# Performance work log

Measured on AMD Instinct MI355X. Metric: run time of the kernel, lower is better.

## Reference

```python
import jax, jax.numpy as jnp
import numpy as np

N_NODES = 100000
N_EDGES = 1600000
IN_FEATS = 256
OUT_FEATS = 128


def setup_inputs() -> dict:
    key = jax.random.key(0)
    k1, k2, k3, k4 = jax.random.split(key, 4)
    feat = jax.random.normal(k1, (N_NODES, IN_FEATS), dtype=jnp.float32)
    src = jax.random.randint(k2, (N_EDGES,), 0, N_NODES, dtype=jnp.int64)
    dst = jax.random.randint(k3, (N_EDGES,), 0, N_NODES, dtype=jnp.int64)
    W = jax.random.normal(k4, (IN_FEATS, OUT_FEATS), dtype=jnp.float32) * (1.0 / np.sqrt(IN_FEATS))
    b = jnp.zeros((OUT_FEATS,), dtype=jnp.float32)
    return {"feat": feat, "src": src, "dst": dst, "W": W, "b": b}


def reference(feat, src, dst, W, b):
    # norm = 'both': symmetric degree normalization, clip degrees at 1
    ones = jnp.ones((src.shape[0],), dtype=jnp.float32)
    out_deg = jax.ops.segment_sum(ones, src, num_segments=N_NODES)  # out-degree per src node
    in_deg = jax.ops.segment_sum(ones, dst, num_segments=N_NODES)   # in-degree per dst node
    norm_src = jnp.power(jnp.clip(out_deg, 1.0, None), -0.5)[:, None]  # (N,1)
    norm_dst = jnp.power(jnp.clip(in_deg, 1.0, None), -0.5)[:, None]   # (N,1)

    h = feat * norm_src
    # in_feats (256) > out_feats (128): apply W before aggregation
    h = h @ W  # (N, out_feats)
    # copy_src + sum aggregation over edges (SpMM)
    msgs = h[src]  # (E, out_feats)
    rst = jax.ops.segment_sum(msgs, dst, num_segments=N_NODES)  # (N, out_feats)
    rst = rst * norm_dst
    rst = rst + b
    return rst
```

## Files before the change

kernel.cpp:

```cpp
#include <hip/hip_runtime.h>
#include <hip/hip_bf16.h>
#include <cstddef>

#define NN 100000
#define NE 1600000
#define INF 256
#define OUTF 128
#define NBKT 196
#define BSH 9
#define P1B 250
#define EPB 6400
#define SCL (NBKT * P1B)
#define SCLP 49152

typedef __bf16 bf16x8 __attribute__((ext_vector_type(8)));
typedef float f32x4 __attribute__((ext_vector_type(4)));

__device__ __forceinline__ float bflo(uint v) { return __uint_as_float(v << 16); }
__device__ __forceinline__ float bfhi(uint v) { return __uint_as_float(v & 0xffff0000u); }

__global__ __launch_bounds__(256) void k_p1a(const int* __restrict__ src,
                                             const int* __restrict__ dst,
                                             int* __restrict__ ghd,
                                             int* __restrict__ ghs,
                                             const float* __restrict__ W,
                                             __bf16* __restrict__ Wt) {
  if (blockIdx.x >= P1B) {
    int i = (blockIdx.x - P1B) * 256 + threadIdx.x;
    if (i < SCLP - SCL) { ghd[SCL + i] = 0; ghs[SCL + i] = 0; }
    int n = i & 127, k = i >> 7;
    Wt[n * INF + k] = (__bf16)W[k * OUTF + n];
    return;
  }
  __shared__ int lhd[NBKT], lhs[NBKT];
  const int t = threadIdx.x;
  if (t < NBKT) { lhd[t] = 0; lhs[t] = 0; }
  __syncthreads();
  const int base = blockIdx.x * EPB;
#pragma unroll
  for (int i = 0; i < EPB / 256; ++i) {
    int e = base + i * 256 + t;
    atomicAdd(&lhd[dst[e] >> BSH], 1);
    atomicAdd(&lhs[src[e] >> BSH], 1);
  }
  __syncthreads();
  if (t < NBKT) {
    ghd[t * P1B + blockIdx.x] = lhd[t];
    ghs[t * P1B + blockIdx.x] = lhs[t];
  }
}

__global__ __launch_bounds__(1024) void k_p1b(int* __restrict__ ghd,
                                              int* __restrict__ ghs,
                                              int* __restrict__ row_start) {
  int* a = blockIdx.x ? ghs : ghd;
  __shared__ int wsum[16];
  const int t = threadIdx.x;
  const int lane = t & 63, wid = t >> 6;
  int4 v[12];
  const int4* p = (const int4*)(a + t * 48);
#pragma unroll
  for (int i = 0; i < 12; ++i) v[i] = p[i];
  int s = 0;
#pragma unroll
  for (int i = 0; i < 12; ++i) s += v[i].x + v[i].y + v[i].z + v[i].w;
  const int mysum = s;
#pragma unroll
  for (int d = 1; d < 64; d <<= 1) {
    int u = __shfl_up(s, d);
    if (lane >= d) s += u;
  }
  if (lane == 63) wsum[wid] = s;
  __syncthreads();
  if (wid == 0) {
    int ws = (lane < 16) ? wsum[lane] : 0;
    int inc = ws;
#pragma unroll
    for (int d = 1; d < 16; d <<= 1) {
      int u = __shfl_up(inc, d);
      if (lane >= d) inc += u;
    }
    if (lane < 16) wsum[lane] = inc - ws;
  }
  __syncthreads();
  int ex = wsum[wid] + s - mysum;
#pragma unroll
  for (int i = 0; i < 12; ++i) {
    int4 w;
    w.x = ex; ex += v[i].x;
    w.y = ex; ex += v[i].y;
    w.z = ex; ex += v[i].z;
    w.w = ex; ex += v[i].w;
    ((int4*)(a + t * 48))[i] = w;
  }
  if (blockIdx.x == 0 && t == 0) row_start[NN] = NE;
}

__global__ __launch_bounds__(256) void k_p1c(const int* __restrict__ src,
                                             const int* __restrict__ dst,
                                             const int* __restrict__ ghd,
                                             const int* __restrict__ ghs,
                                             uint* __restrict__ rec_d,
                                             ushort* __restrict__ rec_s) {
  __shared__ int od[NBKT], os[NBKT];
  const int t = threadIdx.x;
  if (t < NBKT) {
    od[t] = ghd[t * P1B + blockIdx.x];
    os[t] = ghs[t * P1B + blockIdx.x];
  }
  __syncthreads();
  const int base = blockIdx.x * EPB;
#pragma unroll
  for (int i = 0; i < EPB / 256; ++i) {
    int e = base + i * 256 + t;
    int s = src[e], d = dst[e];
    int p = atomicAdd(&od[d >> BSH], 1);
    rec_d[p] = ((uint)s << BSH) | (uint)(d & 511);
    int q = atomicAdd(&os[s >> BSH], 1);
    rec_s[q] = (ushort)(s & 511);
  }
}

__global__ __launch_bounds__(256) void k_p2(const int* __restrict__ ghd,
                                            const int* __restrict__ ghs,
                                            const uint* __restrict__ rec_d,
                                            const ushort* __restrict__ rec_s,
                                            int* __restrict__ edge_src,
                                            int* __restrict__ row_start,
                                            float* __restrict__ ns) {
  __shared__ int lh[512];
  __shared__ int sc[256];
  const int k = blockIdx.x, t = threadIdx.x;
  {
    const int base = ghd[k * P1B];
    const int end = (k == NBKT - 1) ? NE : ghd[(k + 1) * P1B];
    lh[t] = 0; lh[t + 256] = 0;
    __syncthreads();
    for (int j = base + t; j < end; j += 256) atomicAdd(&lh[rec_d[j] & 511], 1);
    __syncthreads();
    int a0 = lh[2 * t], a1 = lh[2 * t + 1];
    sc[t] = a0 + a1;
    __syncthreads();
    for (int off = 1; off < 256; off <<= 1) {
      int add = (t >= off) ? sc[t - off] : 0;
      __syncthreads();
      sc[t] += add;
      __syncthreads();
    }
    int ex = t ? sc[t - 1] : 0;
    int e0 = ex, e1 = ex + a0;
    int n0 = k * 512 + 2 * t;
    if (n0 < NN) row_start[n0] = base + e0;
    if (n0 + 1 < NN) row_start[n0 + 1] = base + e1;
    __syncthreads();
    lh[2 * t] = base + e0;
    lh[2 * t + 1] = base + e1;
    __syncthreads();
    for (int j = base + t; j < end; j += 256) {
      uint r = rec_d[j];
      int p = atomicAdd(&lh[r & 511], 1);
      edge_src[p] = (int)(r >> BSH);
    }
  }
  __syncthreads();
  {
    const int base = ghs[k * P1B];
    const int end = (k == NBKT - 1) ? NE : ghs[(k + 1) * P1B];
    lh[t] = 0; lh[t + 256] = 0;
    __syncthreads();
    for (int j = base + t; j < end; j += 256) atomicAdd(&lh[rec_s[j]], 1);
    __syncthreads();
    int n0 = k * 512 + t, n1 = n0 + 256;
    if (n0 < NN) { int c = lh[t];       ns[n0] = rsqrtf((float)(c > 1 ? c : 1)); }
    if (n1 < NN) { int c = lh[t + 256]; ns[n1] = rsqrtf((float)(c > 1 ? c : 1)); }
  }
}

__global__ __launch_bounds__(512, 4) void k_gemm(const float* __restrict__ feat,
                                                 const __bf16* __restrict__ Wt,
                                                 const float* __restrict__ ns,
                                                 __bf16* __restrict__ h) {
  __shared__ __attribute__((aligned(16))) char lB[65536];
  const int tid = threadIdx.x;
  const int w = tid >> 6, l = tid & 63;
  const int lr = l & 15, kg = l >> 4;
  const int row0 = blockIdx.x * 128 + w * 16;

#pragma unroll
  for (int i = 0; i < 8; ++i) {
    int c = i * 512 + tid;
    int col = c >> 5, g = c & 31;
    bf16x8 v = *(const bf16x8*)(Wt + (size_t)col * INF + g * 8);
    *(bf16x8*)(lB + col * 512 + ((g ^ (col & 7)) * 16)) = v;
  }
  __syncthreads();

  int r0 = row0 + lr; if (r0 >= NN) r0 = NN - 1;
  const float4* ap4k = (const float4*)(feat + (size_t)r0 * INF) + kg * 2;

  f32x4 acc[8];
#pragma unroll
  for (int j = 0; j < 8; ++j) acc[j] = (f32x4)0.0f;

  const char* bb = lB + lr * 512;
  const int lx = lr & 7;

  float4 buf0[4], buf1[4];
#pragma unroll
  for (int i = 0; i < 4; ++i) {
    buf0[i] = ap4k[i * 8];
    buf1[i] = ap4k[i * 8 + 1];
  }
#pragma unroll
  for (int kk = 0; kk < 8; ++kk) {
    float4 c0 = buf0[kk & 3], c1 = buf1[kk & 3];
    if (kk < 4) {
      buf0[kk & 3] = ap4k[(kk + 4) * 8];
      buf1[kk & 3] = ap4k[(kk + 4) * 8 + 1];
    }
    bf16x8 a;
#pragma unroll
    for (int j = 0; j < 4; ++j) {
      a[j] = (__bf16)c0[j];
      a[4 + j] = (__bf16)c1[j];
    }
#pragma unroll
    for (int nf = 0; nf < 8; ++nf) {
      bf16x8 b = *(const bf16x8*)(bb + nf * 8192 + (((kk * 4 + kg) ^ lx) * 16));
      acc[nf] = __builtin_amdgcn_mfma_f32_16x16x32_bf16(a, b, acc[nf], 0, 0, 0);
    }
  }

#pragma unroll
  for (int r = 0; r < 4; ++r) {
    int row = row0 + kg * 4 + r;
    if (row < NN) {
      float nsv = ns[row];
      __bf16* hp = h + (size_t)row * OUTF + lr;
#pragma unroll
      for (int nf = 0; nf < 8; ++nf)
        hp[nf * 16] = (__bf16)(acc[nf][r] * nsv);
    }
  }
}

__global__ __launch_bounds__(256) void k_aggr(const uint4* __restrict__ h4,
                                              const int* __restrict__ row_start,
                                              const int* __restrict__ edge_src,
                                              const float* __restrict__ bias,
                                              float* __restrict__ out) {
  const int wave = threadIdx.x >> 6;
  const int lane = threadIdx.x & 63;
  const int q = lane >> 4;
  const int cl = lane & 15;
  const int n = blockIdx.x * 4 + wave;
  const int s0 = row_start[n];
  const int s1 = row_start[n + 1];
  const int cnt = s1 - s0;

  float a0 = 0.f, a1 = 0.f, a2 = 0.f, a3 = 0.f, a4 = 0.f, a5 = 0.f, a6 = 0.f, a7 = 0.f;
  for (int j0 = 0; j0 < cnt; j0 += 64) {
    int nb = cnt - j0; if (nb > 64) nb = 64;
    int idv = 0;
    if (lane < nb) idv = edge_src[s0 + j0 + lane];
#pragma unroll 8
    for (int j = 0; j < nb; j += 4) {
      int jj = j + q;
      int e = __shfl(idv, jj);
      if (jj < nb) {
        uint4 v = h4[(size_t)e * 16 + cl];
        a0 += bflo(v.x); a1 += bfhi(v.x);
        a2 += bflo(v.y); a3 += bfhi(v.y);
        a4 += bflo(v.z); a5 += bfhi(v.z);
        a6 += bflo(v.w); a7 += bfhi(v.w);
      }
    }
  }
  a0 += __shfl_xor(a0, 16); a1 += __shfl_xor(a1, 16); a2 += __shfl_xor(a2, 16); a3 += __shfl_xor(a3, 16);
  a4 += __shfl_xor(a4, 16); a5 += __shfl_xor(a5, 16); a6 += __shfl_xor(a6, 16); a7 += __shfl_xor(a7, 16);
  a0 += __shfl_xor(a0, 32); a1 += __shfl_xor(a1, 32); a2 += __shfl_xor(a2, 32); a3 += __shfl_xor(a3, 32);
  a4 += __shfl_xor(a4, 32); a5 += __shfl_xor(a5, 32); a6 += __shfl_xor(a6, 32); a7 += __shfl_xor(a7, 32);

  if (q == 0) {
    float ndv = rsqrtf((float)(cnt > 1 ? cnt : 1));
    const float4* b4 = (const float4*)bias;
    float4 ba = b4[2 * cl], bb = b4[2 * cl + 1];
    float4 o0, o1;
    o0.x = a0 * ndv + ba.x; o0.y = a1 * ndv + ba.y; o0.z = a2 * ndv + ba.z; o0.w = a3 * ndv + ba.w;
    o1.x = a4 * ndv + bb.x; o1.y = a5 * ndv + bb.y; o1.z = a6 * ndv + bb.z; o1.w = a7 * ndv + bb.w;
    float4* op = (float4*)(out + (size_t)n * OUTF);
    op[2 * cl] = o0;
    op[2 * cl + 1] = o1;
  }
}

extern "C" void kernel_launch(void* const* d_in, const int* in_sizes, int n_in,
                              void* d_out, int out_size, void* d_ws, size_t ws_size,
                              hipStream_t stream) {
  const float* feat = (const float*)d_in[0];
  const int* src = (const int*)d_in[1];
  const int* dst = (const int*)d_in[2];
  const float* Wm = (const float*)d_in[3];
  const float* bias = (const float*)d_in[4];
  float* out = (float*)d_out;

  char* ws = (char*)d_ws;
  __bf16* h        = (__bf16*)(ws + 0);
  __bf16* Wt       = (__bf16*)(ws + 25600000);
  int*    ghd      = (int*)(ws + 25665536);
  int*    ghs      = (int*)(ws + 25862144);
  uint*   rec_d    = (uint*)(ws + 26058752);
  ushort* rec_s    = (ushort*)(ws + 32458752);
  int*    edge_src = (int*)(ws + 35658752);
  int*    row_start= (int*)(ws + 42058752);
  float*  ns       = (float*)(ws + 42458768);

  k_p1a<<<P1B + 128, 256, 0, stream>>>(src, dst, ghd, ghs, Wm, Wt);
  k_p1b<<<2, 1024, 0, stream>>>(ghd, ghs, row_start);
  k_p1c<<<P1B, 256, 0, stream>>>(src, dst, ghd, ghs, rec_d, rec_s);
  k_p2<<<NBKT, 256, 0, stream>>>(ghd, ghs, rec_d, rec_s, edge_src, row_start, ns);
  k_gemm<<<(NN + 127) / 128, 512, 0, stream>>>(feat, Wt, ns, h);
  k_aggr<<<NN / 4, 256, 0, stream>>>((const uint4*)h, row_start, edge_src, bias, out);
}
```

Measured before the change: 168.0 us.

## Stage bucketed scatter through LDS for coalesced global writes

```diff
diff --git a/kernel.cpp b/kernel.cpp
--- a/kernel.cpp
+++ b/kernel.cpp
@@ -12,6 +12,7 @@
 #define EPB 6400
 #define SCL (NBKT * P1B)
 #define SCLP 49152
+#define P2CAP 10240
 
 typedef __bf16 bf16x8 __attribute__((ext_vector_type(8)));
 typedef float f32x4 __attribute__((ext_vector_type(4)));
@@ -102,22 +103,88 @@
                                              const int* __restrict__ ghs,
                                              uint* __restrict__ rec_d,
                                              ushort* __restrict__ rec_s) {
-  __shared__ int od[NBKT], os[NBKT];
+  __shared__ int hist[256];
+  __shared__ int off[NBKT];
+  __shared__ int adj[NBKT];
+  __shared__ int sc[256];
+  __shared__ uint d4[EPB];
+  __shared__ unsigned char bkt[EPB];
   const int t = threadIdx.x;
+  const int base = blockIdx.x * EPB;
+
+  hist[t] = 0;
+  __syncthreads();
+#pragma unroll
+  for (int i = 0; i < EPB / 256; ++i)
+    atomicAdd(&hist[dst[base + i * 256 + t] >> BSH], 1);
+  __syncthreads();
+  int hv = hist[t];
+  sc[t] = hv;
+  __syncthreads();
+  for (int o = 1; o < 256; o <<= 1) {
+    int add = (t >= o) ? sc[t - o] : 0;
+    __syncthreads();
+    sc[t] += add;
+    __syncthreads();
+  }
+  int lstart = sc[t] - hv;
   if (t < NBKT) {
-    od[t] = ghd[t * P1B + blockIdx.x];
-    os[t] = ghs[t * P1B + blockIdx.x];
-  }
-  __syncthreads();
-  const int base = blockIdx.x * EPB;
+    off[t] = lstart;
+    adj[t] = ghd[t * P1B + blockIdx.x] - lstart;
+  }
+  __syncthreads();
 #pragma unroll
   for (int i = 0; i < EPB / 256; ++i) {
     int e = base + i * 256 + t;
     int s = src[e], d = dst[e];
-    int p = atomicAdd(&od[d >> BSH], 1);
-    rec_d[p] = ((uint)s << BSH) | (uint)(d & 511);
-    int q = atomicAdd(&os[s >> BSH], 1);
-    rec_s[q] = (ushort)(s & 511);
+    int b = d >> BSH;
+    int p = atomicAdd(&off[b], 1);
+    d4[p] = ((uint)s << BSH) | (uint)(d & 511);
+    bkt[p] = (unsigned char)b;
+  }
+  __syncthreads();
+#pragma unroll
+  for (int i = 0; i < EPB / 256; ++i) {
+    int idx = i * 256 + t;
+    rec_d[adj[bkt[idx]] + idx] = d4[idx];
+  }
+  __syncthreads();
+
+  hist[t] = 0;
+  __syncthreads();
+#pragma unroll
+  for (int i = 0; i < EPB / 256; ++i)
+    atomicAdd(&hist[src[base + i * 256 + t] >> BSH], 1);
+  __syncthreads();
+  hv = hist[t];
+  sc[t] = hv;
+  __syncthreads();
+  for (int o = 1; o < 256; o <<= 1) {
+    int add = (t >= o) ? sc[t - o] : 0;
+    __syncthreads();
+    sc[t] += add;
+    __syncthreads();
+  }
+  lstart = sc[t] - hv;
+  if (t < NBKT) {
+    off[t] = lstart;
+    adj[t] = ghs[t * P1B + blockIdx.x] - lstart;
+  }
+  __syncthreads();
+  ushort* s2 = (ushort*)d4;
+#pragma unroll
+  for (int i = 0; i < EPB / 256; ++i) {
+    int s = src[base + i * 256 + t];
+    int b = s >> BSH;
+    int p = atomicAdd(&off[b], 1);
+    s2[p] = (ushort)(s & 511);
+    bkt[p] = (unsigned char)b;
+  }
+  __syncthreads();
+#pragma unroll
+  for (int i = 0; i < EPB / 256; ++i) {
+    int idx = i * 256 + t;
+    rec_s[adj[bkt[idx]] + idx] = s2[idx];
   }
 }
 
@@ -130,10 +197,12 @@
                                             float* __restrict__ ns) {
   __shared__ int lh[512];
   __shared__ int sc[256];
+  __shared__ int lbuf[P2CAP];
   const int k = blockIdx.x, t = threadIdx.x;
   {
     const int base = ghd[k * P1B];
     const int end = (k == NBKT - 1) ? NE : ghd[(k + 1) * P1B];
+    const int cnt = end - base;
     lh[t] = 0; lh[t + 256] = 0;
     __syncthreads();
     for (int j = base + t; j < end; j += 256) atomicAdd(&lh[rec_d[j] & 511], 1);
@@ -153,13 +222,24 @@
     if (n0 < NN) row_start[n0] = base + e0;
     if (n0 + 1 < NN) row_start[n0 + 1] = base + e1;
     __syncthreads();
-    lh[2 * t] = base + e0;
-    lh[2 * t + 1] = base + e1;
-    __syncthreads();
-    for (int j = base + t; j < end; j += 256) {
-      uint r = rec_d[j];
-      int p = atomicAdd(&lh[r & 511], 1);
-      edge_src[p] = (int)(r >> BSH);
+    lh[2 * t] = e0;
+    lh[2 * t + 1] = e1;
+    __syncthreads();
+    if (cnt <= P2CAP) {
+      for (int j = base + t; j < end; j += 256) {
+        uint r = rec_d[j];
+        int p = atomicAdd(&lh[r & 511], 1);
+        lbuf[p] = (int)(r >> BSH);
+      }
+      __syncthreads();
+      for (int i = t; i < cnt; i += 256)
+        edge_src[base + i] = lbuf[i];
+    } else {
+      for (int j = base + t; j < end; j += 256) {
+        uint r = rec_d[j];
+        int p = atomicAdd(&lh[r & 511], 1);
+        edge_src[base + p] = (int)(r >> BSH);
+      }
     }
   }
   __syncthreads();
```

Measured after the change: 165.1 us (median of 2 runs). About the same (-1.7%).
